# Performance work log

Measured on AMD Instinct MI355X. Metric: run time of the kernel, lower is better.

The kernel has to match this reference:

```python
import jax, jax.numpy as jnp
import numpy as np

EPSILON = 0.1
NUM_STAB = 1e-4


def setup_inputs() -> dict:
    key = jax.random.key(0)
    k1, k2, k3 = jax.random.split(key, 3)
    B, C, H, Wd = 1024, 3, 32, 32
    n = C * H * Wd          # 3072 input dims
    c = 10                  # classes
    data = jax.random.normal(k1, (B, C, H, Wd), dtype=jnp.float32)
    # stand-in differentiable classifier (linear) so the Jacobian wrt data is defined
    W = jax.random.normal(k2, (n, c), dtype=jnp.float32) * 0.02
    b = jax.random.normal(k3, (c,), dtype=jnp.float32) * 0.02
    return {"data": data, "W": W, "b": b}


def reference(data, W, b):
    B = data.shape[0]
    n = data.shape[1] * data.shape[2] * data.shape[3]
    c = W.shape[1]
    m = c - 1

    def new_coord_fn(x):  # x: [C,H,W] single sample
        logits = x.reshape(-1) @ W + b                              # [c]
        probs = jax.nn.softmax(logits) * (1 - c * NUM_STAB) + NUM_STAB
        r = jnp.sqrt(probs)
        return 2.0 * r[:m] / (1.0 - r[m])                           # [m]

    # batched Jacobian replaces the per-class autograd.grad loop: [B, m, C, H, W]
    jac = jax.vmap(jax.jacrev(new_coord_fn))(data).reshape(B, m, n)
    G = jnp.einsum('bik,bjk->bij', jac, jac)                        # [B, m, m]

    logits = data.reshape(B, -1) @ W + b                            # [B, c]
    probs = jax.nn.softmax(logits, axis=1) * (1 - c * NUM_STAB) + NUM_STAB
    coeff = 4.0 * (1.0 - jnp.sqrt(probs[:, m])) ** 2                # [B]
    delta = 2.0 * jnp.arccos(jnp.sqrt(probs / c).sum(axis=1))       # [B]
    factor = (delta ** 2 / coeff / EPSILON ** 2)[:, None, None]     # [B,1,1]

    diff = G - factor * jnp.eye(m, dtype=G.dtype)[None]
    reg = jnp.linalg.norm(diff.reshape(B, -1), axis=1) / n          # [B]
    return (reg.mean(), jnp.array(0))
```

## Files before the change

### kernel.cpp

```cpp
#include <hip/hip_runtime.h>
#include <math.h>

#define NDIM   3072
#define C10    10
#define M9     9
#define SYM55  55
#define SPB    4
#define KPT    12


__global__ __launch_bounds__(256) void wtw_kernel(const float* __restrict__ W,
                                                  float* __restrict__ Msym) {
    const int t = threadIdx.x;
    float acc[SYM55];
#pragma unroll
    for (int i = 0; i < SYM55; ++i) acc[i] = 0.f;

    const float4* Wq = (const float4*)(W + (long)t * (KPT * C10));

#pragma unroll 1
    for (int c = 0; c < 3; ++c) {
        float w[40];
#pragma unroll
        for (int p = 0; p < 10; ++p) {
            float4 v = Wq[10 * c + p];
            w[4 * p + 0] = v.x; w[4 * p + 1] = v.y; w[4 * p + 2] = v.z; w[4 * p + 3] = v.w;
        }
#pragma unroll
        for (int kk = 0; kk < 4; ++kk) {
            int idx = 0;
#pragma unroll
            for (int a = 0; a < C10; ++a)
#pragma unroll
                for (int b = a; b < C10; ++b) {
                    acc[idx] = fmaf(w[kk * 10 + a], w[kk * 10 + b], acc[idx]);
                    ++idx;
                }
        }
    }
#pragma unroll
    for (int off = 32; off >= 1; off >>= 1) {
#pragma unroll
        for (int i = 0; i < SYM55; ++i) acc[i] += __shfl_xor(acc[i], off);
    }
    __shared__ float red[4][SYM55];
    const int wid = t >> 6, lane = t & 63;
    if (lane == 0) {
#pragma unroll
        for (int i = 0; i < SYM55; ++i) red[wid][i] = acc[i];
    }
    __syncthreads();
    if (t < SYM55) Msym[t] = red[0][t] + red[1][t] + red[2][t] + red[3][t];
}

__global__ __launch_bounds__(256) void iso_kernel(const float* __restrict__ data,
                                                  const float* __restrict__ W,
                                                  const float* __restrict__ bias,
                                                  const float* __restrict__ Msym,
                                                  float* __restrict__ partials,
                                                  int B) {
    __shared__ float s_red[4][SPB * C10];
    __shared__ float s_M[C10 * C10];
    __shared__ float s_logit[SPB][C10];
    __shared__ float s_p[SPB][C10];
    __shared__ float s_r[SPB][C10];
    __shared__ float s_u[SPB];
    __shared__ float s_fac[SPB];
    __shared__ float s_A[SPB][M9 * C10];
    __shared__ float s_T[SPB][M9 * C10];
    __shared__ float s_sq[SPB][M9 * M9];
    __shared__ float s_part[SPB];

    const int t = threadIdx.x;
    const int sbase = blockIdx.x * SPB;

    const float4* Wq = (const float4*)(W + (long)t * (KPT * C10));
    const float4* xq[SPB];
#pragma unroll
    for (int s = 0; s < SPB; ++s) {
        int sidx = sbase + s; if (sidx >= B) sidx = B - 1;
        xq[s] = (const float4*)(data + (long)sidx * NDIM + (long)t * KPT);
    }

    float acc[SPB][C10];
#pragma unroll
    for (int s = 0; s < SPB; ++s)
#pragma unroll
        for (int j = 0; j < C10; ++j) acc[s][j] = 0.f;

#pragma unroll 1
    for (int c = 0; c < 3; ++c) {
        float w[40];
#pragma unroll
        for (int p = 0; p < 10; ++p) {
            float4 v = Wq[10 * c + p];
            w[4 * p + 0] = v.x; w[4 * p + 1] = v.y; w[4 * p + 2] = v.z; w[4 * p + 3] = v.w;
        }
        float x[SPB][4];
#pragma unroll
        for (int s = 0; s < SPB; ++s) {
            float4 v = xq[s][c];
            x[s][0] = v.x; x[s][1] = v.y; x[s][2] = v.z; x[s][3] = v.w;
        }
#pragma unroll
        for (int kk = 0; kk < 4; ++kk)
#pragma unroll
            for (int s = 0; s < SPB; ++s)
#pragma unroll
                for (int j = 0; j < C10; ++j)
                    acc[s][j] = fmaf(x[s][kk], w[kk * 10 + j], acc[s][j]);
    }

#pragma unroll
    for (int off = 32; off >= 1; off >>= 1) {
#pragma unroll
        for (int s = 0; s < SPB; ++s)
#pragma unroll
            for (int j = 0; j < C10; ++j) acc[s][j] += __shfl_xor(acc[s][j], off);
    }
    const int wid = t >> 6, lane = t & 63;
    if (lane == 0) {
#pragma unroll
        for (int s = 0; s < SPB; ++s)
#pragma unroll
            for (int j = 0; j < C10; ++j) s_red[wid][s * C10 + j] = acc[s][j];
    }
    __syncthreads();

    if (t < SPB * C10) {
        float v = s_red[0][t] + s_red[1][t] + s_red[2][t] + s_red[3][t];
        s_logit[t / C10][t % C10] = v + bias[t % C10];
    }
    if (t >= 64 && t < 64 + SYM55) {
        int e = t - 64;
        int a = 0, rem = e;
        while (rem >= C10 - a) { rem -= C10 - a; ++a; }
        int b = a + rem;
        float v = Msym[e];
        s_M[a * C10 + b] = v;
        s_M[b * C10 + a] = v;
    }
    __syncthreads();

    if (t < SPB) {
        float lg[C10];
#pragma unroll
        for (int j = 0; j < C10; ++j) lg[j] = s_logit[t][j];
        float mx = lg[0];
#pragma unroll
        for (int j = 1; j < C10; ++j) mx = fmaxf(mx, lg[j]);
        float ex[C10], sum = 0.f;
#pragma unroll
        for (int j = 0; j < C10; ++j) { ex[j] = expf(lg[j] - mx); sum += ex[j]; }
        float inv = 1.f / sum;
        float ssq = 0.f;
#pragma unroll
        for (int j = 0; j < C10; ++j) {
            float p = ex[j] * inv;
            float q = fmaf(p, 0.999f, 1e-4f);
            float r = sqrtf(q);
            s_p[t][j] = p;
            s_r[t][j] = r;
            ssq += sqrtf(q * 0.1f);
        }
        ssq = fminf(ssq, 1.0f);
        float delta = 2.f * acosf(ssq);
        float rm = s_r[t][M9];
        float omr = 1.f - rm;
        float u = 1.f / omr;
        float coeff = 4.f * omr * omr;
        s_u[t] = u;
        s_fac[t] = delta * delta / (coeff * (0.1f * 0.1f));
    }
    __syncthreads();

    for (int e = t; e < SPB * M9 * C10; e += 256) {
        int s = e / (M9 * C10), rem = e % (M9 * C10);
        int i = rem / C10, j = rem % C10;
        float u = s_u[s];
        float pi = s_p[s][i], ri = s_r[s][i];
        float p9 = s_p[s][M9], r9 = s_r[s][M9];
        float alpha = u * 0.999f * pi / ri;
        float beta  = u * u * 0.999f * ri * p9 / r9;
        float a = -(alpha + beta) * s_p[s][j];
        if (j == i)  a += alpha;
        if (j == M9) a += beta;
        s_A[s][rem] = a;
    }
    __syncthreads();

    for (int e = t; e < SPB * M9 * C10; e += 256) {
        int s = e / (M9 * C10), rem = e % (M9 * C10);
        int i = rem / C10, b = rem % C10;
        float sum = 0.f;
#pragma unroll
        for (int j = 0; j < C10; ++j) sum = fmaf(s_A[s][i * C10 + j], s_M[j * C10 + b], sum);
        s_T[s][rem] = sum;
    }
    __syncthreads();

    for (int e = t; e < SPB * M9 * M9; e += 256) {
        int s = e / (M9 * M9), rem = e % (M9 * M9);
        int i = rem / M9, k = rem % M9;
        float g = 0.f;
#pragma unroll
        for (int b = 0; b < C10; ++b) g = fmaf(s_T[s][i * C10 + b], s_A[s][k * C10 + b], g);
        float d = g - ((i == k) ? s_fac[s] : 0.f);
        s_sq[s][rem] = d * d;
    }
    __syncthreads();

    if (t < SPB) {
        int sidx = sbase + t;
        float sum = 0.f;
#pragma unroll
        for (int r = 0; r < M9 * M9; ++r) sum += s_sq[t][r];
        s_part[t] = (sidx < B) ? sqrtf(sum) : 0.f;
    }
    __syncthreads();
    if (t == 0) {
        partials[blockIdx.x] = (s_part[0] + s_part[1] + s_part[2] + s_part[3]) * (1.0f / NDIM);
    }
}

__global__ __launch_bounds__(256) void finalize_kernel(const float* __restrict__ partials,
                                                       float* __restrict__ out,
                                                       int nb, float invB, int out_size) {
    const int t = threadIdx.x;
    float v = 0.f;
    for (int i = t; i < nb; i += 256) v += partials[i];
#pragma unroll
    for (int off = 32; off >= 1; off >>= 1) v += __shfl_xor(v, off);
    __shared__ float red[4];
    const int wid = t >> 6, lane = t & 63;
    if (lane == 0) red[wid] = v;
    __syncthreads();
    if (t == 0) {
        out[0] = (red[0] + red[1] + red[2] + red[3]) * invB;
        if (out_size > 1) out[1] = 0.f;
    }
}

extern "C" void kernel_launch(void* const* d_in, const int* in_sizes, int n_in,
                              void* d_out, int out_size, void* d_ws, size_t ws_size,
                              hipStream_t stream) {
    const float* data = (const float*)d_in[0];
    const float* W    = (const float*)d_in[1];
    const float* bias = (const float*)d_in[2];
    float* out  = (float*)d_out;
    float* ws   = (float*)d_ws;
    const int B = in_sizes[0] / NDIM;
    const int nblocks = (B + SPB - 1) / SPB;

    wtw_kernel<<<1, 256, 0, stream>>>(W, ws);
    iso_kernel<<<nblocks, 256, 0, stream>>>(data, W, bias, ws, ws + 64, B);
    finalize_kernel<<<1, 256, 0, stream>>>(ws + 64, out, nblocks, 1.0f / (float)B, out_size);
}
```

Before: 83.13 us.

## Transpose W in prep kernel, parallelize WᵀW, fuse finalize via last-block atomic

Replaces the single-block WᵀW kernel with a 32-block prep kernel that computes 12 partial WᵀW sums and also writes a class-major transposed copy of W into the workspace. The main kernel reads the transposed W and the data with fully coalesced float4 strided accesses instead of per-thread contiguous 48-element chunks. The separate finalize kernel is removed: the last block to finish, found with an atomic counter, performs the final reduction. This saves a launch and improves coalescing, at the cost of an extra transposed-W write and read each call and atomic traffic.

```diff
diff --git a/kernel.cpp b/kernel.cpp
--- a/kernel.cpp
+++ b/kernel.cpp
@@ -6,61 +6,65 @@
 #define M9     9
 #define SYM55  55
 #define SPB    4
-#define KPT    12
-
-
-__global__ __launch_bounds__(256) void wtw_kernel(const float* __restrict__ W,
-                                                  float* __restrict__ Msym) {
-    const int t = threadIdx.x;
-    float acc[SYM55];
-#pragma unroll
-    for (int i = 0; i < SYM55; ++i) acc[i] = 0.f;
-
-    const float4* Wq = (const float4*)(W + (long)t * (KPT * C10));
-
-#pragma unroll 1
-    for (int c = 0; c < 3; ++c) {
-        float w[40];
-#pragma unroll
-        for (int p = 0; p < 10; ++p) {
-            float4 v = Wq[10 * c + p];
-            w[4 * p + 0] = v.x; w[4 * p + 1] = v.y; w[4 * p + 2] = v.z; w[4 * p + 3] = v.w;
-        }
-#pragma unroll
-        for (int kk = 0; kk < 4; ++kk) {
-            int idx = 0;
-#pragma unroll
-            for (int a = 0; a < C10; ++a)
-#pragma unroll
-                for (int b = a; b < C10; ++b) {
-                    acc[idx] = fmaf(w[kk * 10 + a], w[kk * 10 + b], acc[idx]);
-                    ++idx;
-                }
-        }
-    }
-#pragma unroll
-    for (int off = 32; off >= 1; off >>= 1) {
-#pragma unroll
-        for (int i = 0; i < SYM55; ++i) acc[i] += __shfl_xor(acc[i], off);
-    }
-    __shared__ float red[4][SYM55];
-    const int wid = t >> 6, lane = t & 63;
-    if (lane == 0) {
-#pragma unroll
-        for (int i = 0; i < SYM55; ++i) red[wid][i] = acc[i];
-    }
-    __syncthreads();
-    if (t < SYM55) Msym[t] = red[0][t] + red[1][t] + red[2][t] + red[3][t];
+
+#define MPART_OFF 64
+#define WT_OFF    1024
+#define PART_OFF  (WT_OFF + C10 * NDIM)
+
+__global__ __launch_bounds__(256) void prep_kernel(const float* __restrict__ W,
+                                                   float* __restrict__ ws) {
+    const int t = threadIdx.x, b = blockIdx.x;
+    if (b == 0 && t == 0) ((unsigned int*)ws)[0] = 0u;
+
+    const int g = b * 256 + t;
+    if (g < (NDIM * C10) / 4) {
+        float4 v = ((const float4*)W)[g];
+        float vv[4] = {v.x, v.y, v.z, v.w};
+        const int base = 4 * g;
+#pragma unroll
+        for (int q = 0; q < 4; ++q) {
+            int flat = base + q;
+            int k = flat / C10, j = flat - k * C10;
+            ws[WT_OFF + j * NDIM + k] = vv[q];
+        }
+    }
+
+    if (b < 12) {
+        const int r = b * 256 + t;
+        float w[C10];
+        const float2* row = (const float2*)(W + (long)r * C10);
+#pragma unroll
+        for (int p = 0; p < 5; ++p) { float2 v2 = row[p]; w[2*p] = v2.x; w[2*p+1] = v2.y; }
+        float acc[SYM55];
+        int idx = 0;
+#pragma unroll
+        for (int a = 0; a < C10; ++a)
+#pragma unroll
+            for (int c = a; c < C10; ++c) { acc[idx] = w[a] * w[c]; ++idx; }
+#pragma unroll
+        for (int off = 32; off >= 1; off >>= 1) {
+#pragma unroll
+            for (int i = 0; i < SYM55; ++i) acc[i] += __shfl_xor(acc[i], off);
+        }
+        __shared__ float red[4][SYM55];
+        const int wid = t >> 6, lane = t & 63;
+        if (lane == 0) {
+#pragma unroll
+            for (int i = 0; i < SYM55; ++i) red[wid][i] = acc[i];
+        }
+        __syncthreads();
+        if (t < SYM55)
+            ws[MPART_OFF + b * 64 + t] = red[0][t] + red[1][t] + red[2][t] + red[3][t];
+    }
 }
 
 __global__ __launch_bounds__(256) void iso_kernel(const float* __restrict__ data,
-                                                  const float* __restrict__ W,
                                                   const float* __restrict__ bias,
-                                                  const float* __restrict__ Msym,
-                                                  float* __restrict__ partials,
-                                                  int B) {
+                                                  float* ws,
+                                                  float* __restrict__ out,
+                                                  int B, float invB, int out_size) {
+    __shared__ float s_M[C10 * C10];
     __shared__ float s_red[4][SPB * C10];
-    __shared__ float s_M[C10 * C10];
     __shared__ float s_logit[SPB][C10];
     __shared__ float s_p[SPB][C10];
     __shared__ float s_r[SPB][C10];
@@ -70,45 +74,54 @@
     __shared__ float s_T[SPB][M9 * C10];
     __shared__ float s_sq[SPB][M9 * M9];
     __shared__ float s_part[SPB];
+    __shared__ int s_last;
 
     const int t = threadIdx.x;
     const int sbase = blockIdx.x * SPB;
 
-    const float4* Wq = (const float4*)(W + (long)t * (KPT * C10));
-    const float4* xq[SPB];
+    if (t < SYM55) {
+        float v = 0.f;
+#pragma unroll
+        for (int i = 0; i < 12; ++i) v += ws[MPART_OFF + i * 64 + t];
+        int a = 0, rem = t;
+        while (rem >= C10 - a) { rem -= C10 - a; ++a; }
+        int c2 = a + rem;
+        s_M[a * C10 + c2] = v;
+        s_M[c2 * C10 + a] = v;
+    }
+
+    const float* WT = ws + WT_OFF;
+    float x[SPB][12];
 #pragma unroll
     for (int s = 0; s < SPB; ++s) {
         int sidx = sbase + s; if (sidx >= B) sidx = B - 1;
-        xq[s] = (const float4*)(data + (long)sidx * NDIM + (long)t * KPT);
-    }
-
+        const float4* xq = (const float4*)(data + (long)sidx * NDIM);
+#pragma unroll
+        for (int i = 0; i < 3; ++i) {
+            float4 v = xq[t + 256 * i];
+            x[s][4*i+0] = v.x; x[s][4*i+1] = v.y; x[s][4*i+2] = v.z; x[s][4*i+3] = v.w;
+        }
+    }
     float acc[SPB][C10];
 #pragma unroll
     for (int s = 0; s < SPB; ++s)
 #pragma unroll
         for (int j = 0; j < C10; ++j) acc[s][j] = 0.f;
 
-#pragma unroll 1
-    for (int c = 0; c < 3; ++c) {
-        float w[40];
-#pragma unroll
-        for (int p = 0; p < 10; ++p) {
-            float4 v = Wq[10 * c + p];
-            w[4 * p + 0] = v.x; w[4 * p + 1] = v.y; w[4 * p + 2] = v.z; w[4 * p + 3] = v.w;
-        }
-        float x[SPB][4];
-#pragma unroll
-        for (int s = 0; s < SPB; ++s) {
-            float4 v = xq[s][c];
-            x[s][0] = v.x; x[s][1] = v.y; x[s][2] = v.z; x[s][3] = v.w;
-        }
-#pragma unroll
-        for (int kk = 0; kk < 4; ++kk)
-#pragma unroll
-            for (int s = 0; s < SPB; ++s)
-#pragma unroll
-                for (int j = 0; j < C10; ++j)
-                    acc[s][j] = fmaf(x[s][kk], w[kk * 10 + j], acc[s][j]);
+#pragma unroll
+    for (int j = 0; j < C10; ++j) {
+        const float4* wtj = (const float4*)(WT + (long)j * NDIM);
+#pragma unroll
+        for (int i = 0; i < 3; ++i) {
+            float4 wv = wtj[t + 256 * i];
+#pragma unroll
+            for (int s = 0; s < SPB; ++s) {
+                acc[s][j] = fmaf(x[s][4*i+0], wv.x, acc[s][j]);
+                acc[s][j] = fmaf(x[s][4*i+1], wv.y, acc[s][j]);
+                acc[s][j] = fmaf(x[s][4*i+2], wv.z, acc[s][j]);
+                acc[s][j] = fmaf(x[s][4*i+3], wv.w, acc[s][j]);
+            }
+        }
     }
 
 #pragma unroll
@@ -130,15 +143,6 @@
     if (t < SPB * C10) {
         float v = s_red[0][t] + s_red[1][t] + s_red[2][t] + s_red[3][t];
         s_logit[t / C10][t % C10] = v + bias[t % C10];
-    }
-    if (t >= 64 && t < 64 + SYM55) {
-        int e = t - 64;
-        int a = 0, rem = e;
-        while (rem >= C10 - a) { rem -= C10 - a; ++a; }
-        int b = a + rem;
-        float v = Msym[e];
-        s_M[a * C10 + b] = v;
-        s_M[b * C10 + a] = v;
     }
     __syncthreads();
 
@@ -218,26 +222,28 @@
         s_part[t] = (sidx < B) ? sqrtf(sum) : 0.f;
     }
     __syncthreads();
+
     if (t == 0) {
-        partials[blockIdx.x] = (s_part[0] + s_part[1] + s_part[2] + s_part[3]) * (1.0f / NDIM);
-    }
-}
-
-__global__ __launch_bounds__(256) void finalize_kernel(const float* __restrict__ partials,
-                                                       float* __restrict__ out,
-                                                       int nb, float invB, int out_size) {
-    const int t = threadIdx.x;
-    float v = 0.f;
-    for (int i = t; i < nb; i += 256) v += partials[i];
-#pragma unroll
-    for (int off = 32; off >= 1; off >>= 1) v += __shfl_xor(v, off);
-    __shared__ float red[4];
-    const int wid = t >> 6, lane = t & 63;
-    if (lane == 0) red[wid] = v;
-    __syncthreads();
-    if (t == 0) {
-        out[0] = (red[0] + red[1] + red[2] + red[3]) * invB;
-        if (out_size > 1) out[1] = 0.f;
+        float part = (s_part[0] + s_part[1] + s_part[2] + s_part[3]) * (1.0f / NDIM);
+        atomicExch(&ws[PART_OFF + blockIdx.x], part);
+        __threadfence();
+        unsigned int old = atomicAdd((unsigned int*)ws, 1u);
+        s_last = (old == gridDim.x - 1) ? 1 : 0;
+    }
+    __syncthreads();
+
+    if (s_last) {
+        float v = 0.f;
+        for (int i = t; i < (int)gridDim.x; i += 256)
+            v += atomicAdd(&ws[PART_OFF + i], 0.f);
+#pragma unroll
+        for (int off = 32; off >= 1; off >>= 1) v += __shfl_xor(v, off);
+        if (lane == 0) s_red[wid][0] = v;
+        __syncthreads();
+        if (t == 0) {
+            out[0] = (s_red[0][0] + s_red[1][0] + s_red[2][0] + s_red[3][0]) * invB;
+            if (out_size > 1) out[1] = 0.f;
+        }
     }
 }
 
@@ -247,12 +253,11 @@
     const float* data = (const float*)d_in[0];
     const float* W    = (const float*)d_in[1];
     const float* bias = (const float*)d_in[2];
-    float* out  = (float*)d_out;
-    float* ws   = (float*)d_ws;
+    float* out = (float*)d_out;
+    float* ws  = (float*)d_ws;
     const int B = in_sizes[0] / NDIM;
     const int nblocks = (B + SPB - 1) / SPB;
 
-    wtw_kernel<<<1, 256, 0, stream>>>(W, ws);
-    iso_kernel<<<nblocks, 256, 0, stream>>>(data, W, bias, ws, ws + 64, B);
-    finalize_kernel<<<1, 256, 0, stream>>>(ws + 64, out, nblocks, 1.0f / (float)B, out_size);
+    prep_kernel<<<32, 256, 0, stream>>>(W, ws);
+    iso_kernel<<<nblocks, 256, 0, stream>>>(data, bias, ws, out, B, 1.0f / (float)B, out_size);
 }
```

After: 83.02 us. No clear change (-0.1%).
